# Kernel tuning notes

Measured on AMD Instinct MI355X. Metric: run time of the kernel, lower is better.

The kernel has to match this reference:

```python
import jax, jax.numpy as jnp
import numpy as np

EPS = 1e-6
H, KV, D = 16, 4, 128  # num_heads, num_kv_heads, head_dim
ROPE_BASE = 1000000.0


def rmsnorm(x, w):
    # weight_offset = 1.0: scale is (w + 1)
    var = jnp.mean(x * x, axis=-1, keepdims=True)
    return x * jax.lax.rsqrt(var + EPS) * (w + 1.0)


def rope_tables(S, dtype):
    inv_freq = 1.0 / (ROPE_BASE ** (np.arange(0, D, 2, dtype=np.float32) / D))
    freqs = np.outer(np.arange(S, dtype=np.float32), inv_freq)  # [S, D/2]
    emb = np.concatenate([freqs, freqs], axis=-1)  # [S, D]
    return jnp.asarray(np.cos(emb), dtype), jnp.asarray(np.sin(emb), dtype)


def rotate_half(x):
    x1, x2 = jnp.split(x, 2, axis=-1)
    return jnp.concatenate([-x2, x1], axis=-1)


def setup_inputs() -> dict:
    key = jax.random.key(0)
    ks = jax.random.split(key, 5)
    B, S, HID = 2, 2048, 2048
    return {
        "x": jax.random.normal(ks[0], (B, S, HID), jnp.float32),
        "Wq": jax.random.normal(ks[1], (HID, 2 * H * D), jnp.float32) * 0.02,
        "Wk": jax.random.normal(ks[2], (HID, KV * D), jnp.float32) * 0.02,
        "Wv": jax.random.normal(ks[3], (HID, KV * D), jnp.float32) * 0.02,
        "Wo": jax.random.normal(ks[4], (H * D, HID), jnp.float32) * 0.02,
        "qn_w": jnp.zeros((D,), jnp.float32),
        "kn_w": jnp.zeros((D,), jnp.float32),
    }


def reference(x, Wq, Wk, Wv, Wo, qn_w, kn_w):
    B, S, _ = x.shape
    G = H // KV  # GQA group size
    # projections
    q_raw = (x @ Wq).reshape(B, S, H, 2 * D)
    q, gate = q_raw[..., :D], q_raw[..., D:]
    k = (x @ Wk).reshape(B, S, KV, D)
    v = (x @ Wv).reshape(B, S, KV, D)
    # QK RMSNorm (per head_dim)
    q = rmsnorm(q, qn_w)
    k = rmsnorm(k, kn_w)
    # RoPE (rotate-half form)
    cos, sin = rope_tables(S, x.dtype)  # [S, D]
    c = cos[None, :, None, :]
    s = sin[None, :, None, :]
    q = q * c + rotate_half(q) * s
    k = k * c + rotate_half(k) * s
    # grouped attention: avoid materializing repeated K/V
    # q: [B,S,H,D] -> [B,KV,G,S,D]; head h = kv*G + g matches repeat_interleave
    qg = q.transpose(0, 2, 1, 3).reshape(B, KV, G, S, D)
    kt = k.transpose(0, 2, 1, 3)  # [B,KV,S,D]
    vt = v.transpose(0, 2, 1, 3)  # [B,KV,S,D]
    scale = 1.0 / np.sqrt(D)
    scores = jnp.einsum("bkgsd,bktd->bkgst", qg, kt) * scale  # [B,KV,G,S,S]
    causal = jnp.tril(jnp.ones((S, S), bool))
    scores = jnp.where(causal, scores, jnp.finfo(scores.dtype).min)
    probs = jax.nn.softmax(scores, axis=-1)
    out = jnp.einsum("bkgst,bktd->bkgsd", probs, vt)  # [B,KV,G,S,D]
    out = out.reshape(B, H, S, D)
    # sigmoid gating from q projection
    gate = gate.transpose(0, 2, 1, 3)  # [B,H,S,D]
    out = out * jax.nn.sigmoid(gate)
    out = out.transpose(0, 2, 1, 3).reshape(B, S, H * D)
    return out @ Wo
```

## Files before the change

kernel.cpp:

```cpp
#include <hip/hip_runtime.h>
#include <hip/hip_bf16.h>

typedef unsigned short u16;
typedef __bf16 bf16x8 __attribute__((ext_vector_type(8)));
typedef float f32x4 __attribute__((ext_vector_type(4)));
typedef float f32x16 __attribute__((ext_vector_type(16)));

#define B_   2
#define S_   2048
#define HID_ 2048
#define H_   16
#define KV_  4
#define D_   128
#define TS_  5120

template <int V> struct ic { static constexpr int value = V; };

__device__ __forceinline__ u16 f2b(float f) {
  unsigned u = __float_as_uint(f);
  return (u16)((u + 0x7fffu + ((u >> 16) & 1u)) >> 16);
}
__device__ __forceinline__ float b2f(u16 h) {
  return __uint_as_float(((unsigned)h) << 16);
}
__device__ __forceinline__ unsigned pk2(float a, float b) {
  __hip_bfloat162 h = __float22bfloat162_rn(make_float2(a, b));
  unsigned u;
  __builtin_memcpy(&u, &h, 4);
  return u;
}
__device__ __forceinline__ void cstore(float* p, float v) { *p = v; }
__device__ __forceinline__ void cstore(u16* p, float v)   { *p = f2b(v); }

__device__ __forceinline__ void gl_lds16(const u16* g, u16* l) {
  __builtin_amdgcn_global_load_lds(
      (const __attribute__((address_space(1))) unsigned int*)g,
      (__attribute__((address_space(3))) unsigned int*)l, 16, 0, 0);
}


__global__ __launch_bounds__(256)
void cast_f2b_kernel(const float* __restrict__ in, u16* __restrict__ out) {
  const int idx = blockIdx.x * 256 + threadIdx.x;
  const int r = idx >> 8;
  const int k = (idx & 255) << 3;
  const float4 v0 = *(const float4*)(in + (size_t)r * 2048 + k);
  const float4 v1 = *(const float4*)(in + (size_t)r * 2048 + k + 4);
  uint4 w;
  w.x = pk2(v0.x, v0.y); w.y = pk2(v0.z, v0.w);
  w.z = pk2(v1.x, v1.y); w.w = pk2(v1.z, v1.w);
  const size_t off =
      ((((size_t)(r >> 4) * 64 + (k >> 5)) * 64) + ((k >> 3) & 3) * 16 +
       (r & 15)) * 8;
  *(uint4*)(out + off) = w;
}

__global__ __launch_bounds__(256)
void transpose_w_kernel(const float* __restrict__ in, u16* __restrict__ out,
                        int R, int Cc) {
  __shared__ u16 t[32][33];
  const int tx = threadIdx.x, ty = threadIdx.y;
  const int c0 = blockIdx.x * 32, r0 = blockIdx.y * 32;
#pragma unroll
  for (int i = 0; i < 4; i++)
    t[ty + i * 8][tx] = f2b(in[(size_t)(r0 + ty + i * 8) * Cc + c0 + tx]);
  __syncthreads();
  const int tid = ty * 32 + tx;
  if (tid < 128) {
    const int tl = tid >> 6, l = tid & 63, li = l & 15, quad = l >> 4;
    u16 vals[8];
#pragma unroll
    for (int e = 0; e < 8; e++) vals[e] = t[quad * 8 + e][tl * 16 + li];
    const size_t off =
        ((((size_t)(c0 >> 4) + tl) * (R >> 5) + (r0 >> 5)) * 64 + quad * 16 +
         li) * 8;
    *(uint4*)(out + off) = *(const uint4*)vals;
  }
}

__global__ __launch_bounds__(256)
void transpose_v_kernel(const u16* __restrict__ in, u16* __restrict__ out,
                        int tokstride) {
  __shared__ u16 t[32][33];
  const int tx = threadIdx.x, ty = threadIdx.y;
  const int jt = blockIdx.x, dt = blockIdx.y;
  const int s0 = jt * 32, d0 = dt * 32;
  const int z = blockIdx.z, b = z >> 2, kv = z & 3;
#pragma unroll
  for (int i = 0; i < 4; i++)
    t[ty + i * 8][tx] =
        in[(size_t)(b * S_ + s0 + ty + i * 8) * tokstride + kv * D_ + d0 + tx];
  __syncthreads();
  const int tid = ty * 32 + tx;
  if (tid < 128) {
    const int kk = tid >> 6, hi2 = (tid >> 5) & 1, d31 = tid & 31;
    u16 vals[8];
#pragma unroll
    for (int e = 0; e < 8; e++) vals[e] = t[kk * 16 + hi2 * 8 + e][d31];
    const size_t off =
        ((((size_t)(b * KV_ + kv) * 64 + jt) * 8 + dt * 2 + kk) * 64 +
         hi2 * 32 + d31) * 8;
    *(uint4*)(out + off) = *(const uint4*)vals;
  }
}

template <typename CT>
__global__ __launch_bounds__(256)
void gemm_nt(const u16* __restrict__ A, const u16* __restrict__ Bt,
             CT* __restrict__ C, int Md, int Nd, int Kd) {
  __shared__ u16 As[8 * 512];
  __shared__ u16 Bs[8 * 512];
  const int tid = threadIdx.x;
  const int lane = tid & 63;
  const int wave = tid >> 6;
  const int wm = wave >> 1, wn = wave & 1;
  const int li = lane & 15, quad = lane >> 4;
  const int m0 = blockIdx.y * 128;
  const int n0 = blockIdx.x * 128;

  f32x4 acc[4][4];
#pragma unroll
  for (int i = 0; i < 4; i++)
#pragma unroll
    for (int j = 0; j < 4; j++) acc[i][j] = (f32x4){0.f, 0.f, 0.f, 0.f};

  const size_t ts = (size_t)(Kd >> 5) * 512;
  const u16* Ab = A + ((size_t)(m0 >> 4) + wave * 2) * ts + lane * 8;
  const u16* Bb = Bt + ((size_t)(n0 >> 4) + wave * 2) * ts + lane * 8;
  u16* Al0 = &As[(wave * 2) * 512];
  u16* Al1 = &As[(wave * 2 + 1) * 512];
  u16* Bl0 = &Bs[(wave * 2) * 512];
  u16* Bl1 = &Bs[(wave * 2 + 1) * 512];

  for (int k0 = 0; k0 < Kd; k0 += 32) {
    const size_t ko = (size_t)k0 * 16;
    __syncthreads();
    gl_lds16(Ab + ko, Al0);
    gl_lds16(Ab + ts + ko, Al1);
    gl_lds16(Bb + ko, Bl0);
    gl_lds16(Bb + ts + ko, Bl1);
    __syncthreads();
    bf16x8 af[4], bfr[4];
#pragma unroll
    for (int mt = 0; mt < 4; mt++)
      af[mt] = *(const bf16x8*)&As[(wm * 4 + mt) * 512 + lane * 8];
#pragma unroll
    for (int nt = 0; nt < 4; nt++)
      bfr[nt] = *(const bf16x8*)&Bs[(wn * 4 + nt) * 512 + lane * 8];
#pragma unroll
    for (int mt = 0; mt < 4; mt++)
#pragma unroll
      for (int nt = 0; nt < 4; nt++)
        acc[mt][nt] = __builtin_amdgcn_mfma_f32_16x16x32_bf16(
            af[mt], bfr[nt], acc[mt][nt], 0, 0, 0);
  }
#pragma unroll
  for (int mt = 0; mt < 4; mt++) {
    const int row = m0 + wm * 64 + mt * 16 + quad * 4;
#pragma unroll
    for (int nt = 0; nt < 4; nt++) {
      const int col = n0 + wn * 64 + nt * 16 + li;
#pragma unroll
      for (int r = 0; r < 4; r++)
        cstore(&C[(size_t)(row + r) * Nd + col], acc[mt][nt][r]);
    }
  }
}

__global__ __launch_bounds__(256)
void rmsrope_kernel(const u16* __restrict__ in, const float* __restrict__ w,
                    u16* __restrict__ out, int n_heads, int tok_stride,
                    int head_stride, float scale) {
  const int warp = (blockIdx.x << 2) + (threadIdx.x >> 6);
  const int lane = threadIdx.x & 63;
  const int h = warp % n_heads;
  const int tok = warp / n_heads;
  const int s = tok & (S_ - 1);
  const int b = tok >> 11;
  const u16* src = in + (size_t)tok * tok_stride + (size_t)h * head_stride;
  float x1 = b2f(src[lane]);
  float x2 = b2f(src[lane + 64]);
  float ss = x1 * x1 + x2 * x2;
#pragma unroll
  for (int off = 1; off < 64; off <<= 1) ss += __shfl_xor(ss, off);
  const float inv = rsqrtf(ss * (1.0f / 128.0f) + 1e-6f) * scale;
  x1 *= inv * (w[lane] + 1.0f);
  x2 *= inv * (w[lane + 64] + 1.0f);
  const float invf = exp2f((float)lane * (-19.931568569324174f / 64.0f));
  const float ang = (float)s * invf;
  float sn, c;
  sincosf(ang, &sn, &c);
  const int wq = lane >> 4, hi = (lane >> 3) & 1, e = lane & 7;
  const size_t tb = (((size_t)b * n_heads + h) * 64 + (s >> 5)) * 4096;
  const size_t o1 = tb + (size_t)(wq * 64 + hi * 32 + (s & 31)) * 8 + e;
  out[o1]        = f2b(x1 * c - x2 * sn);
  out[o1 + 2048] = f2b(x2 * c + x1 * sn);
}

__global__ __launch_bounds__(128, 2)
void attn_kernel(const u16* __restrict__ Q, const u16* __restrict__ Kr,
                 const u16* __restrict__ Vt, const u16* __restrict__ qraw,
                 u16* __restrict__ Ag) {
  __shared__ __align__(16) float Wscr[2][2176];
  __shared__ float Mdump[2][32], Ldump[2][32];

  const int tid = threadIdx.x;
  const int lane = tid & 63;
  const int wv = tid >> 6;
  const int l31 = lane & 31, hi = lane >> 5;

  const int id = blockIdx.x;
  const int grp = id & 7;
  const int b = grp >> 2, kv = grp & 3;
  const int rest = id >> 3;
  const int hh = rest & 3;
  const int t = 63 - (rest >> 2);
  const int h = (kv << 2) | hh;
  const int bh = (b << 4) | h;
  const int rs = t * 32;

  const u16* Qb = Q + ((size_t)bh * 64 + t) * 4096;
  const u16* Kb = Kr + (size_t)(b * KV_ + kv) * 64 * 4096;
  const u16* Vb = Vt + (size_t)(b * KV_ + kv) * 64 * 4096;

  bf16x8 qf[8];
#pragma unroll
  for (int w = 0; w < 8; w++)
    qf[w] = *(const bf16x8*)(Qb + w * 512 + lane * 8);

  float m_s = -1e30f, l_s = 0.f;
  f32x16 oacc[4];
#pragma unroll
  for (int dt = 0; dt < 4; dt++)
#pragma unroll
    for (int i = 0; i < 16; i++) oacc[dt][i] = 0.f;

  const int h0 = (t + 2) >> 1;
  const int klo = wv ? h0 : 0;
  const int khi = wv ? (t + 1) : h0;

  bf16x8 kf[8];
  auto loadK = [&](int jt) {
    const u16* kp = Kb + (size_t)jt * 4096 + lane * 8;
#pragma unroll
    for (int w = 0; w < 8; w++) kf[w] = *(const bf16x8*)(kp + w * 512);
  };

  auto step = [&](int jt) {
    const u16* vp = Vb + (size_t)jt * 4096 + lane * 8;
    bf16x8 vf[8];
#pragma unroll
    for (int f = 0; f < 8; f++)
      vf[f] = *(const bf16x8*)(vp + f * 512);

    f32x16 s0, s1;
#pragma unroll
    for (int i = 0; i < 16; i++) { s0[i] = 0.f; s1[i] = 0.f; }
#pragma unroll
    for (int dc = 0; dc < 4; dc++) {
      s0 = __builtin_amdgcn_mfma_f32_32x32x16_bf16(kf[2 * dc], qf[2 * dc], s0,
                                                   0, 0, 0);
      s1 = __builtin_amdgcn_mfma_f32_32x32x16_bf16(kf[2 * dc + 1],
                                                   qf[2 * dc + 1], s1, 0, 0, 0);
    }
    if (jt + 1 < khi) loadK(jt + 1);
    f32x16 s = s0 + s1;

    if (jt == t) {
#pragma unroll
      for (int r = 0; r < 16; r++) {
        const int kl = (r & 3) + 8 * (r >> 2) + 4 * hi;
        if (kl > l31) s[r] = -1e30f;
      }
    }
    float mx4[4];
#pragma unroll
    for (int g = 0; g < 4; g++)
      mx4[g] = fmaxf(fmaxf(s[4 * g], s[4 * g + 1]),
                     fmaxf(s[4 * g + 2], s[4 * g + 3]));
    float mx = fmaxf(fmaxf(mx4[0], mx4[1]), fmaxf(mx4[2], mx4[3]));
    mx = fmaxf(mx, __shfl_xor(mx, 32));
    const bool defer = __all(mx - m_s <= 8.f);
    const float mn = defer ? m_s : fmaxf(m_s, mx);
    if (!defer) {
      const float alpha = __expf(m_s - mn);
      m_s = mn;
      l_s *= alpha;
#pragma unroll
      for (int dt = 0; dt < 4; dt++)
#pragma unroll
        for (int i = 0; i < 16; i++) oacc[dt][i] *= alpha;
    }
    float rs4[4];
#pragma unroll
    for (int g = 0; g < 4; g++) {
      float e0 = __expf(s[4 * g + 0] - mn);
      float e1 = __expf(s[4 * g + 1] - mn);
      float e2 = __expf(s[4 * g + 2] - mn);
      float e3 = __expf(s[4 * g + 3] - mn);
      s[4 * g + 0] = e0; s[4 * g + 1] = e1;
      s[4 * g + 2] = e2; s[4 * g + 3] = e3;
      rs4[g] = (e0 + e1) + (e2 + e3);
    }
    float rsum = (rs4[0] + rs4[1]) + (rs4[2] + rs4[3]);
    rsum += __shfl_xor(rsum, 32);
    l_s += rsum;
    unsigned a0 = pk2(s[0], s[1]),  b0 = pk2(s[2], s[3]);
    unsigned c0 = pk2(s[4], s[5]),  d0 = pk2(s[6], s[7]);
    unsigned e0 = pk2(s[8], s[9]),  f0 = pk2(s[10], s[11]);
    unsigned g0 = pk2(s[12], s[13]), h0w = pk2(s[14], s[15]);
    unsigned r1 = __shfl_xor(hi ? a0 : c0, 32);
    unsigned r2 = __shfl_xor(hi ? b0 : d0, 32);
    unsigned r3 = __shfl_xor(hi ? e0 : g0, 32);
    unsigned r4 = __shfl_xor(hi ? f0 : h0w, 32);
    union U16B { unsigned u[4]; bf16x8 v; };
    U16B p0, p1;
    p0.u[0] = hi ? r1 : a0;  p0.u[1] = hi ? r2 : b0;
    p0.u[2] = hi ? c0 : r1;  p0.u[3] = hi ? d0 : r2;
    p1.u[0] = hi ? r3 : e0;  p1.u[1] = hi ? r4 : f0;
    p1.u[2] = hi ? g0 : r3;  p1.u[3] = hi ? h0w : r4;
#pragma unroll
    for (int dt = 0; dt < 4; dt++) {
      oacc[dt] = __builtin_amdgcn_mfma_f32_32x32x16_bf16(vf[dt * 2], p0.v,
                                                         oacc[dt], 0, 0, 0);
      oacc[dt] = __builtin_amdgcn_mfma_f32_32x32x16_bf16(vf[dt * 2 + 1], p1.v,
                                                         oacc[dt], 0, 0, 0);
    }
  };

  if (klo < khi) {
    loadK(klo);
    for (int jt = klo; jt < khi; jt++) step(jt);
  }

  float* myscr = &Wscr[wv][0];
  auto dumpO = [&](auto wvc) {
    constexpr int WV = decltype(wvc)::value;
#pragma unroll
    for (int i = 0; i < 2; i++) {
#pragma unroll
      for (int g = 0; g < 4; g++) {
        f32x4 w;
        w[0] = oacc[(1 - WV) * 2 + i][4 * g + 0];
        w[1] = oacc[(1 - WV) * 2 + i][4 * g + 1];
        w[2] = oacc[(1 - WV) * 2 + i][4 * g + 2];
        w[3] = oacc[(1 - WV) * 2 + i][4 * g + 3];
        *(f32x4*)&myscr[l31 * 68 + i * 32 + 8 * g + 4 * hi] = w;
      }
    }
    if (hi == 0) {
      Mdump[WV][l31] = m_s;
      Ldump[WV][l31] = l_s;
    }
  };
  if (wv == 0) dumpO(ic<0>{}); else dumpO(ic<1>{});
  __syncthreads();
  auto finO = [&](auto wvc) {
    constexpr int WV = decltype(wvc)::value;
    const float* oscr = &Wscr[1 - WV][0];
    const float mo = Mdump[1 - WV][l31];
    const float lo2 = Ldump[1 - WV][l31];
    const float mm = fmaxf(m_s, mo);
    const float as = __expf(m_s - mm), ao = __expf(mo - mm);
    const float linv = 1.f / (l_s * as + lo2 * ao);
    const size_t tok = (size_t)b * S_ + rs + l31;
    const u16* gp = qraw + tok * TS_ + h * 256 + 128;
#pragma unroll
    for (int i = 0; i < 2; i++) {
#pragma unroll
      for (int g = 0; g < 4; g++) {
        const int dbase = (WV * 2 + i) * 32 + 8 * g + 4 * hi;
        const int dg = h * 128 + dbase;
        f32x4 oo = *(const f32x4*)&oscr[l31 * 68 + i * 32 + 8 * g + 4 * hi];
        uint2 gv = *(const uint2*)(gp + dbase);
        float g0 = b2f((u16)(gv.x & 0xffff)), g1 = b2f((u16)(gv.x >> 16));
        float g2 = b2f((u16)(gv.y & 0xffff)), g3 = b2f((u16)(gv.y >> 16));
        float o0 = (oacc[WV * 2 + i][4 * g + 0] * as + oo[0] * ao) * linv /
                   (1.f + __expf(-g0));
        float o1 = (oacc[WV * 2 + i][4 * g + 1] * as + oo[1] * ao) * linv /
                   (1.f + __expf(-g1));
        float o2 = (oacc[WV * 2 + i][4 * g + 2] * as + oo[2] * ao) * linv /
                   (1.f + __expf(-g2));
        float o3 = (oacc[WV * 2 + i][4 * g + 3] * as + oo[3] * ao) * linv /
                   (1.f + __expf(-g3));
        const size_t off =
            (((tok >> 4) * 64 + (dg >> 5)) * 64 + ((dg >> 3) & 3) * 16 +
             (tok & 15)) * 8 + 4 * hi;
        *(uint2*)(Ag + off) = make_uint2(pk2(o0, o1), pk2(o2, o3));
      }
    }
  };
  if (wv == 0) finO(ic<0>{}); else finO(ic<1>{});
}

extern "C" void kernel_launch(void* const* d_in, const int* in_sizes, int n_in,
                              void* d_out, int out_size, void* d_ws,
                              size_t ws_size, hipStream_t stream) {
  const float* x  = (const float*)d_in[0];
  const float* Wq = (const float*)d_in[1];
  const float* Wk = (const float*)d_in[2];
  const float* Wv = (const float*)d_in[3];
  const float* Wo = (const float*)d_in[4];
  const float* qn = (const float*)d_in[5];
  const float* kn = (const float*)d_in[6];
  float* out = (float*)d_out;
  char* ws = (char*)d_ws;

  u16* xb    = (u16*)(ws + 0);
  u16* Wqt   = (u16*)(ws + 16777216);
  u16* Wkvt  = (u16*)(ws + 33554432);
  u16* Wot   = (u16*)(ws + 37748736);
  u16* qkraw = (u16*)(ws + 46137344);
  u16* Vtb   = (u16*)(ws + 88080384);
  u16* Kr    = (u16*)(ws + 92274688);
  u16* Ag    = (u16*)(ws + 96468992);
  u16* Qr = xb;

  cast_f2b_kernel<<<4096, 256, 0, stream>>>(x, xb);
  transpose_w_kernel<<<dim3(128, 64), dim3(32, 8), 0, stream>>>(Wq, Wqt, 2048, 4096);
  transpose_w_kernel<<<dim3(16, 64), dim3(32, 8), 0, stream>>>(Wk, Wkvt, 2048, 512);
  transpose_w_kernel<<<dim3(16, 64), dim3(32, 8), 0, stream>>>(Wv, Wkvt + 512 * 2048,
                                                               2048, 512);
  transpose_w_kernel<<<dim3(64, 64), dim3(32, 8), 0, stream>>>(Wo, Wot, 2048, 2048);

  gemm_nt<u16><<<dim3(40, 32), 256, 0, stream>>>(xb, Wqt, qkraw, 4096, TS_, 2048);

  rmsrope_kernel<<<16384, 256, 0, stream>>>(qkraw, qn, Qr, 16, TS_, 256,
                                            0.08838834764831845f);
  rmsrope_kernel<<<4096, 256, 0, stream>>>(qkraw + 4096, kn, Kr, 4, TS_, 128,
                                           1.0f);
  transpose_v_kernel<<<dim3(64, 4, 8), dim3(32, 8), 0, stream>>>(
      qkraw + 4096 + 512, Vtb, TS_);

  attn_kernel<<<2048, 128, 0, stream>>>(Qr, Kr, Vtb, qkraw, Ag);
  gemm_nt<float><<<dim3(16, 32), 256, 0, stream>>>(Ag, Wot, out, 4096, 2048, 2048);
}
```

Before: 397.1 us.

## Double-buffer GEMM LDS tiles and remap blocks for XCD-local L2 reuse

The GEMM kernel now uses two LDS buffers per operand. It issues global-to-LDS loads for the next K slice before computing on the current one, which removes one barrier per iteration and overlaps loads with MFMA work. Launches switch to a 1D grid, and block ids are remapped so that each group of blocks sharing id mod 8 covers a contiguous band of N tiles across all M tiles, aiming for better L2 locality per XCD. This doubles LDS use per block, which may reduce occupancy. The remap hardcodes 32 M tiles and assumes Nd is a multiple of 1024.

After: 382.2 us. 3.8% less time.

```diff
diff --git a/kernel.cpp b/kernel.cpp
--- a/kernel.cpp
+++ b/kernel.cpp
@@ -108,15 +108,20 @@
 __global__ __launch_bounds__(256)
 void gemm_nt(const u16* __restrict__ A, const u16* __restrict__ Bt,
              CT* __restrict__ C, int Md, int Nd, int Kd) {
-  __shared__ u16 As[8 * 512];
-  __shared__ u16 Bs[8 * 512];
+  __shared__ u16 As[2][8 * 512];
+  __shared__ u16 Bs[2][8 * 512];
   const int tid = threadIdx.x;
   const int lane = tid & 63;
   const int wave = tid >> 6;
   const int wm = wave >> 1, wn = wave & 1;
   const int li = lane & 15, quad = lane >> 4;
-  const int m0 = blockIdx.y * 128;
-  const int n0 = blockIdx.x * 128;
+
+  const int id = blockIdx.x;
+  const int grp = id & 7;
+  const int r = id >> 3;
+  const int px = Nd >> 10;
+  const int m0 = (r & 31) * 128;
+  const int n0 = (grp * px + (r >> 5)) * 128;
 
   f32x4 acc[4][4];
 #pragma unroll
@@ -127,32 +132,34 @@
   const size_t ts = (size_t)(Kd >> 5) * 512;
   const u16* Ab = A + ((size_t)(m0 >> 4) + wave * 2) * ts + lane * 8;
   const u16* Bb = Bt + ((size_t)(n0 >> 4) + wave * 2) * ts + lane * 8;
-  u16* Al0 = &As[(wave * 2) * 512];
-  u16* Al1 = &As[(wave * 2 + 1) * 512];
-  u16* Bl0 = &Bs[(wave * 2) * 512];
-  u16* Bl1 = &Bs[(wave * 2 + 1) * 512];
-
+
+  auto stage = [&](int buf, int k0) {
+    const size_t ko = (size_t)k0 * 16;
+    gl_lds16(Ab + ko, &As[buf][(wave * 2) * 512]);
+    gl_lds16(Ab + ts + ko, &As[buf][(wave * 2 + 1) * 512]);
+    gl_lds16(Bb + ko, &Bs[buf][(wave * 2) * 512]);
+    gl_lds16(Bb + ts + ko, &Bs[buf][(wave * 2 + 1) * 512]);
+  };
+
+  stage(0, 0);
+  int cur = 0;
   for (int k0 = 0; k0 < Kd; k0 += 32) {
-    const size_t ko = (size_t)k0 * 16;
     __syncthreads();
-    gl_lds16(Ab + ko, Al0);
-    gl_lds16(Ab + ts + ko, Al1);
-    gl_lds16(Bb + ko, Bl0);
-    gl_lds16(Bb + ts + ko, Bl1);
-    __syncthreads();
+    if (k0 + 32 < Kd) stage(cur ^ 1, k0 + 32);
     bf16x8 af[4], bfr[4];
 #pragma unroll
     for (int mt = 0; mt < 4; mt++)
-      af[mt] = *(const bf16x8*)&As[(wm * 4 + mt) * 512 + lane * 8];
+      af[mt] = *(const bf16x8*)&As[cur][(wm * 4 + mt) * 512 + lane * 8];
 #pragma unroll
     for (int nt = 0; nt < 4; nt++)
-      bfr[nt] = *(const bf16x8*)&Bs[(wn * 4 + nt) * 512 + lane * 8];
+      bfr[nt] = *(const bf16x8*)&Bs[cur][(wn * 4 + nt) * 512 + lane * 8];
 #pragma unroll
     for (int mt = 0; mt < 4; mt++)
 #pragma unroll
       for (int nt = 0; nt < 4; nt++)
         acc[mt][nt] = __builtin_amdgcn_mfma_f32_16x16x32_bf16(
             af[mt], bfr[nt], acc[mt][nt], 0, 0, 0);
+    cur ^= 1;
   }
 #pragma unroll
   for (int mt = 0; mt < 4; mt++) {
@@ -161,8 +168,8 @@
     for (int nt = 0; nt < 4; nt++) {
       const int col = n0 + wn * 64 + nt * 16 + li;
 #pragma unroll
-      for (int r = 0; r < 4; r++)
-        cstore(&C[(size_t)(row + r) * Nd + col], acc[mt][nt][r]);
+      for (int r2 = 0; r2 < 4; r2++)
+        cstore(&C[(size_t)(row + r2) * Nd + col], acc[mt][nt][r2]);
     }
   }
 }
@@ -423,7 +430,7 @@
                                                                2048, 512);
   transpose_w_kernel<<<dim3(64, 64), dim3(32, 8), 0, stream>>>(Wo, Wot, 2048, 2048);
 
-  gemm_nt<u16><<<dim3(40, 32), 256, 0, stream>>>(xb, Wqt, qkraw, 4096, TS_, 2048);
+  gemm_nt<u16><<<1280, 256, 0, stream>>>(xb, Wqt, qkraw, 4096, TS_, 2048);
 
   rmsrope_kernel<<<16384, 256, 0, stream>>>(qkraw, qn, Qr, 16, TS_, 256,
                                             0.08838834764831845f);
@@ -433,5 +440,5 @@
       qkraw + 4096 + 512, Vtb, TS_);
 
   attn_kernel<<<2048, 128, 0, stream>>>(Qr, Kr, Vtb, qkraw, Ag);
-  gemm_nt<float><<<dim3(16, 32), 256, 0, stream>>>(Ag, Wot, out, 4096, 2048, 2048);
-}
+  gemm_nt<float><<<512, 256, 0, stream>>>(Ag, Wot, out, 4096, 2048, 2048);
+}
```
